# Kernel tuning notes

Measured on AMD Instinct MI355X. Metric: run time of the kernel, lower is better.

Reference implementation:

```python
import jax, jax.numpy as jnp
import numpy as np

N_NODES = 50000
N_EDGES = 800000
IN_DIM = 128
OUT_DIM = 128
NEG_INIT = -1e9  # matches torch fill_(-1e9) init for scatter amax
LEAKY_SLOPE = 0.01  # nn.LeakyReLU default


def setup_inputs() -> dict:
    key = jax.random.key(0)
    ks = jax.random.split(key, 8)
    x = jax.random.normal(ks[0], (N_NODES, IN_DIM), dtype=jnp.float32)
    edge_index = jax.random.randint(ks[1], (2, N_EDGES), 0, N_NODES, dtype=jnp.int64)
    edge_weight = jax.random.uniform(ks[2], (N_EDGES,), dtype=jnp.float32)
    # MLP params (nn.Linear default init: U(-1/sqrt(fan_in), 1/sqrt(fan_in)))
    s1 = 1.0 / np.sqrt(IN_DIM)
    s2 = 1.0 / np.sqrt(OUT_DIM)
    w1 = jax.random.uniform(ks[3], (OUT_DIM, IN_DIM), minval=-s1, maxval=s1, dtype=jnp.float32)
    b1 = jax.random.uniform(ks[4], (OUT_DIM,), minval=-s1, maxval=s1, dtype=jnp.float32)
    w2 = jax.random.uniform(ks[5], (OUT_DIM, OUT_DIM), minval=-s2, maxval=s2, dtype=jnp.float32)
    b2 = jax.random.uniform(ks[6], (OUT_DIM,), minval=-s2, maxval=s2, dtype=jnp.float32)
    eps = jnp.zeros((1,), dtype=jnp.float32)
    return {"x": x, "edge_index": edge_index, "edge_weight": edge_weight,
            "w1": w1, "b1": b1, "w2": w2, "b2": b2, "eps": eps}


def reference(x, edge_index, edge_weight, w1, b1, w2, b2, eps):
    src = edge_index[0]
    dst = edge_index[1]
    # gather + optional edge-weight scale: [E, D]
    messages = x[src] * edge_weight[:, None]
    # scatter-max to dst; init at -1e9 so include_self=False semantics hold
    agg = jnp.full(x.shape, NEG_INIT, dtype=x.dtype).at[dst].max(messages)
    agg = jnp.where(agg == NEG_INIT, jnp.zeros_like(agg), agg)  # isolated nodes -> 0
    h = (1.0 + eps) * x + agg  # eps broadcasts ([1])
    h = h @ w1.T + b1
    h = jnp.where(h >= 0, h, LEAKY_SLOPE * h)  # LeakyReLU
    out = h @ w2.T + b2
    return out
```

## Files before the change

kernel.cpp:

```cpp
#include <hip/hip_runtime.h>
#include <stdint.h>

#define NN 50000
#define NE 800000
#define D  128
#define CAP 64
#define OVF_CAP 131072

#define CNT_OFF     64
#define OVF_CNT_OFF (CNT_OFF + NN)
#define OVF_OFF     (OVF_CNT_OFF + 4)
#define BKT_OFF     312320
#define XH_OFF      (BKT_OFF + NN * CAP)
#define WH_OFF      (XH_OFF + 65536 * (D / 2))

#define HSTRIDE 136

#define FILL_BLKS 3125
#define PX_BLKS   6250
#define PW_BLKS   32

typedef _Float16 half8 __attribute__((ext_vector_type(8)));
typedef __attribute__((ext_vector_type(4))) float float4v;

__device__ __forceinline__ float b2f(uint16_t u) {
    union { uint32_t u; float f; } v; v.u = ((uint32_t)u) << 16; return v.f;
}
__device__ __forceinline__ uint16_t f2b(float f) {
    union { float f; uint32_t u; } v; v.f = f;
    uint32_t r = v.u + 0x7fffu + ((v.u >> 16) & 1u);
    return (uint16_t)(r >> 16);
}
__device__ __forceinline__ ushort f2h(float f) {
    union { _Float16 h; ushort u; } v; v.h = (_Float16)f; return v.u;
}
__device__ __forceinline__ float h2f(ushort u) {
    union { ushort u; _Float16 h; } v; v.u = u; return (float)v.h;
}

__device__ __forceinline__ void block_probe(const uint16_t* __restrict__ xraw,
                                            const int* __restrict__ eraw,
                                            int* sflags) {
    int t = threadIdx.x;
    if (t < 64) {
        float v0 = b2f(xraw[2 * t]);
        float v1 = b2f(xraw[2 * t + 1]);
        int bad = (!(v0 > -1e4f && v0 < 1e4f)) || (!(v1 > -1e4f && v1 < 1e4f));
        unsigned long long bm = __ballot(bad);
        int nz = (t < 32) ? (eraw[2 * t + 1] != 0) : 0;
        unsigned long long im = __ballot(nz);
        if (t == 0) { sflags[0] = bm ? 1 : 0; sflags[1] = im ? 0 : 1; }
    }
    __syncthreads();
}

__global__ __launch_bounds__(256) void prep_fill_kernel(
    const uint16_t* __restrict__ xraw,
    const int*      __restrict__ eraw,
    const uint16_t* __restrict__ ewraw,
    const uint16_t* __restrict__ w1raw,
    const uint16_t* __restrict__ w2raw,
    int* __restrict__ ws)
{
    __shared__ int sflags[2];
    block_probe(xraw, eraw, sflags);
    const int f32 = sflags[0], i64 = sflags[1];

    int bid = blockIdx.x;
    if (bid < FILL_BLKS) {
        int e = bid * 256 + threadIdx.x;
        int src, dst;
        if (i64) {
            const long long* e64 = (const long long*)eraw;
            src = (int)e64[e];
            dst = (int)e64[NE + e];
        } else {
            src = eraw[e];
            dst = eraw[NE + e];
        }
        if ((unsigned)src >= NN || (unsigned)dst >= NN) return;
        uint w = f32 ? (uint)f2h(((const float*)ewraw)[e]) : (uint)f2h(b2f(ewraw[e]));
        uint entry = (w << 16) | (uint)src;
        int slot = atomicAdd(ws + CNT_OFF + dst, 1) + 1;
        if (slot < CAP) {
            ((uint*)(ws + BKT_OFF))[(size_t)dst * CAP + slot] = entry;
        } else {
            int o = atomicAdd(ws + OVF_CNT_OFF, 1) + 1;
            if (o < OVF_CAP) {
                ws[OVF_OFF + 2 * o]     = dst;
                ws[OVF_OFF + 2 * o + 1] = (int)entry;
            }
        }
    } else if (bid < FILL_BLKS + PX_BLKS) {
        int i4 = ((bid - FILL_BLKS) * 256 + threadIdx.x) * 4;
        ushort* dst = (ushort*)(ws + XH_OFF);
        if (f32) {
            float4 v = *(const float4*)((const float*)xraw + i4);
            ushort4 o; o.x = f2h(v.x); o.y = f2h(v.y); o.z = f2h(v.z); o.w = f2h(v.w);
            *(ushort4*)(dst + i4) = o;
        } else {
            ushort4 v = *(const ushort4*)(xraw + i4);
            ushort4 o; o.x = f2h(b2f(v.x)); o.y = f2h(b2f(v.y));
            o.z = f2h(b2f(v.z)); o.w = f2h(b2f(v.w));
            *(ushort4*)(dst + i4) = o;
        }
    } else {
        int i4 = ((bid - FILL_BLKS - PX_BLKS) * 256 + threadIdx.x) * 4;
        const uint16_t* src = (i4 < 16384) ? w1raw : w2raw;
        int off = i4 & 16383;
        ushort* dst = (ushort*)(ws + WH_OFF);
        if (f32) {
            float4 v = *(const float4*)((const float*)src + off);
            ushort4 o; o.x = f2h(v.x); o.y = f2h(v.y); o.z = f2h(v.z); o.w = f2h(v.w);
            *(ushort4*)(dst + i4) = o;
        } else {
            ushort4 v = *(const ushort4*)(src + off);
            ushort4 o; o.x = f2h(b2f(v.x)); o.y = f2h(b2f(v.y));
            o.z = f2h(b2f(v.z)); o.w = f2h(b2f(v.w));
            *(ushort4*)(dst + i4) = o;
        }
    }
}

__global__ __launch_bounds__(256) void gmlp_kernel(
    const uint16_t* __restrict__ xraw,
    const int*      __restrict__ eraw,
    const uint16_t* __restrict__ b1raw,
    const uint16_t* __restrict__ b2raw,
    const uint16_t* __restrict__ epsraw,
    const int* __restrict__ ws,
    uint16_t* __restrict__ outraw)
{
    __shared__ int    sflags[2];
    __shared__ uint   tl[16 * (HSTRIDE / 2)];
    __shared__ ushort hl[16 * HSTRIDE];

    block_probe(xraw, eraw, sflags);
    const int f32 = sflags[0];

    const int tid  = threadIdx.x;
    const int wave = tid >> 6;
    const int lane = tid & 63;
    const int m    = lane & 15;
    const int quad = lane >> 4;
    const int node0 = blockIdx.x * 16;

    const ushort* w1h = (const ushort*)(ws + WH_OFF);
    const ushort* w2h = w1h + 16384;
    const uint*   xh  = (const uint*)(ws + XH_OFF);
    const uint*   bkt = (const uint*)(ws + BKT_OFF);
    const uint    lane4 = (uint)lane * 4;

    const float eps1 = 1.0f + (f32 ? ((const float*)epsraw)[0] : b2f(epsraw[0]));

    int cr[4];
    #pragma unroll
    for (int j = 0; j < 4; ++j)
        cr[j] = ws[CNT_OFF + node0 + wave * 4 + j];

    for (int j = 0; j < 4; ++j) {
        int nl = wave * 4 + j;
        int n  = node0 + nl;
        int deg = cr[j] + 1;
        int cnt = (deg < CAP) ? deg : CAP;

        uint mm[16];
        #pragma unroll
        for (int u = 0; u < 16; ++u) mm[u] = 0xFFFFFFFFu;

        const uint* brow = bkt + (size_t)n * CAP;
        for (int i = 0; i < cnt; i += 16) {
            uint4 q[4];
            #pragma unroll
            for (int qq = 0; qq < 4; ++qq) q[qq] = *(const uint4*)(brow + i + qq * 4);
            #pragma unroll
            for (int u = 0; u < 16; ++u) {
                uint e0  = ((const uint*)q)[u];
                uint off = ((e0 & 0xffffu) << 8) + lane4;
                uint v   = *(const uint*)((const char*)xh + off);
                uint p;
                asm("v_pk_mul_f16 %0, %1, %2 op_sel:[0,1] op_sel_hi:[1,1]"
                    : "=v"(p) : "v"(v), "v"(e0));
                asm("v_pk_max_f16 %0, %0, %1" : "+v"(mm[u]) : "v"(p));
            }
        }
        #pragma unroll
        for (int u = 8; u > 0; u >>= 1)
            #pragma unroll
            for (int v2 = 0; v2 < u; ++v2)
                asm("v_pk_max_f16 %0, %0, %1" : "+v"(mm[v2]) : "v"(mm[v2 + u]));

        float mx = h2f((ushort)(mm[0] & 0xffffu));
        float my = h2f((ushort)(mm[0] >> 16));

        if (deg > CAP) {
            int novf = ws[OVF_CNT_OFF] + 1;
            if (novf > OVF_CAP) novf = OVF_CAP;
            for (int o = 0; o < novf; ++o) {
                if (ws[OVF_OFF + 2 * o] == n) {
                    uint e0 = (uint)ws[OVF_OFF + 2 * o + 1];
                    uint v  = xh[(e0 & 0xffffu) * 64 + lane];
                    float w = h2f((ushort)(e0 >> 16));
                    mx = fmaxf(mx, h2f((ushort)(v & 0xffffu)) * w);
                    my = fmaxf(my, h2f((ushort)(v >> 16)) * w);
                }
            }
        }
        if (deg == 0) { mx = 0.f; my = 0.f; }

        uint xv = xh[(size_t)n * 64 + lane];
        float t0 = eps1 * h2f((ushort)(xv & 0xffffu)) + mx;
        float t1 = eps1 * h2f((ushort)(xv >> 16)) + my;
        tl[nl * (HSTRIDE / 2) + lane] = (uint)f2h(t0) | ((uint)f2h(t1) << 16);
    }
    __syncthreads();

    half8 a[4];
    {
        const ushort* arow = (const ushort*)tl + m * HSTRIDE + quad * 8;
        #pragma unroll
        for (int kb = 0; kb < 4; ++kb) a[kb] = *(const half8*)(arow + kb * 32);
    }

    #pragma unroll
    for (int t = 0; t < 2; ++t) {
        int ct = wave * 2 + t;
        float4v c = {0.f, 0.f, 0.f, 0.f};
        const ushort* brow = w1h + (size_t)(ct * 16 + m) * 128 + quad * 8;
        #pragma unroll
        for (int kb = 0; kb < 4; ++kb)
            c = __builtin_amdgcn_mfma_f32_16x16x32_f16(a[kb], *(const half8*)(brow + kb * 32), c, 0, 0, 0);
        float bias = f32 ? ((const float*)b1raw)[ct * 16 + m] : b2f(b1raw[ct * 16 + m]);
        #pragma unroll
        for (int r = 0; r < 4; ++r) {
            float v = c[r] + bias;
            v = (v >= 0.f) ? v : 0.01f * v;
            hl[(quad * 4 + r) * HSTRIDE + ct * 16 + m] = f2h(v);
        }
    }
    __syncthreads();

    half8 ah[4];
    {
        const ushort* hrow = hl + m * HSTRIDE + quad * 8;
        #pragma unroll
        for (int kb = 0; kb < 4; ++kb) ah[kb] = *(const half8*)(hrow + kb * 32);
    }

    #pragma unroll
    for (int t = 0; t < 2; ++t) {
        int ct = wave * 2 + t;
        float4v c = {0.f, 0.f, 0.f, 0.f};
        const ushort* brow = w2h + (size_t)(ct * 16 + m) * 128 + quad * 8;
        #pragma unroll
        for (int kb = 0; kb < 4; ++kb)
            c = __builtin_amdgcn_mfma_f32_16x16x32_f16(ah[kb], *(const half8*)(brow + kb * 32), c, 0, 0, 0);
        float bias = f32 ? ((const float*)b2raw)[ct * 16 + m] : b2f(b2raw[ct * 16 + m]);
        #pragma unroll
        for (int r = 0; r < 4; ++r) {
            float v = c[r] + bias;
            size_t o = (size_t)(node0 + quad * 4 + r) * 128 + ct * 16 + m;
            if (f32) ((float*)outraw)[o] = v;
            else     outraw[o] = f2b(v);
        }
    }
}

extern "C" void kernel_launch(void* const* d_in, const int* in_sizes, int n_in,
                              void* d_out, int out_size, void* d_ws, size_t ws_size,
                              hipStream_t stream) {
    const uint16_t* x    = (const uint16_t*)d_in[0];
    const int*      eidx = (const int*)     d_in[1];
    const uint16_t* ew   = (const uint16_t*)d_in[2];
    const uint16_t* w1   = (const uint16_t*)d_in[3];
    const uint16_t* b1   = (const uint16_t*)d_in[4];
    const uint16_t* w2   = (const uint16_t*)d_in[5];
    const uint16_t* b2   = (const uint16_t*)d_in[6];
    const uint16_t* eps  = (const uint16_t*)d_in[7];
    uint16_t*       out  = (uint16_t*)d_out;
    int* ws = (int*)d_ws;

    hipMemsetAsync((char*)d_ws + (size_t)CNT_OFF * 4, 0xFF,
                   (size_t)(BKT_OFF + (size_t)NN * CAP - CNT_OFF) * 4, stream);
    prep_fill_kernel<<<FILL_BLKS + PX_BLKS + PW_BLKS, 256, 0, stream>>>(
        x, eidx, ew, w1, w2, ws);
    gmlp_kernel<<<NN / 16, 256, 0, stream>>>(x, eidx, b1, b2, eps, ws, out);
}
```

Baseline: 195.5 us.

## Shrink workspace memset, batch edge atomics, interleave gathers across four nodes

The memset now clears only the per-node counters and overflow count instead of the whole bucket array. Bucket entries past each node's count are masked in the gather loop, so they no longer need the 0xFF fill. The fill stage now handles four edges per thread with the atomics issued back to back. The aggregation loop gathers bucket entries and x rows for all four nodes of a wave before reducing, which exposes more outstanding loads at the cost of higher register pressure.

```diff
diff --git a/kernel.cpp b/kernel.cpp
--- a/kernel.cpp
+++ b/kernel.cpp
@@ -16,7 +16,7 @@
 
 #define HSTRIDE 136
 
-#define FILL_BLKS 3125
+#define FILL_BLKS 782
 #define PX_BLKS   6250
 #define PW_BLKS   32
 
@@ -68,27 +68,44 @@
 
     int bid = blockIdx.x;
     if (bid < FILL_BLKS) {
-        int e = bid * 256 + threadIdx.x;
-        int src, dst;
-        if (i64) {
-            const long long* e64 = (const long long*)eraw;
-            src = (int)e64[e];
-            dst = (int)e64[NE + e];
-        } else {
-            src = eraw[e];
-            dst = eraw[NE + e];
-        }
-        if ((unsigned)src >= NN || (unsigned)dst >= NN) return;
-        uint w = f32 ? (uint)f2h(((const float*)ewraw)[e]) : (uint)f2h(b2f(ewraw[e]));
-        uint entry = (w << 16) | (uint)src;
-        int slot = atomicAdd(ws + CNT_OFF + dst, 1) + 1;
-        if (slot < CAP) {
-            ((uint*)(ws + BKT_OFF))[(size_t)dst * CAP + slot] = entry;
-        } else {
-            int o = atomicAdd(ws + OVF_CNT_OFF, 1) + 1;
-            if (o < OVF_CAP) {
-                ws[OVF_OFF + 2 * o]     = dst;
-                ws[OVF_OFF + 2 * o + 1] = (int)entry;
+        int ebase = bid * 1024 + threadIdx.x;
+        int dst[4]; uint ent[4]; bool val[4];
+        #pragma unroll
+        for (int k = 0; k < 4; ++k) {
+            int e  = ebase + k * 256;
+            val[k] = (e < NE);
+            int ec = val[k] ? e : 0;
+            int s, d2;
+            if (i64) {
+                const long long* e64 = (const long long*)eraw;
+                s  = (int)e64[ec];
+                d2 = (int)e64[NE + ec];
+            } else {
+                s  = eraw[ec];
+                d2 = eraw[NE + ec];
+            }
+            if ((unsigned)s >= NN || (unsigned)d2 >= NN) val[k] = false;
+            uint w = f32 ? (uint)f2h(((const float*)ewraw)[ec])
+                         : (uint)f2h(b2f(ewraw[ec]));
+            dst[k] = d2;
+            ent[k] = (w << 16) | (uint)(s & 0xffff);
+        }
+        int slot[4];
+        #pragma unroll
+        for (int k = 0; k < 4; ++k) {
+            slot[k] = 0x7fffffff;
+            if (val[k]) slot[k] = atomicAdd(ws + CNT_OFF + dst[k], 1) + 1;
+        }
+        #pragma unroll
+        for (int k = 0; k < 4; ++k) {
+            if (slot[k] < CAP) {
+                ((uint*)(ws + BKT_OFF))[(size_t)dst[k] * CAP + slot[k]] = ent[k];
+            } else if (slot[k] != 0x7fffffff) {
+                int o = atomicAdd(ws + OVF_CNT_OFF, 1) + 1;
+                if (o < OVF_CAP) {
+                    ws[OVF_OFF + 2 * o]     = dst[k];
+                    ws[OVF_OFF + 2 * o + 1] = (int)ent[k];
+                }
             }
         }
     } else if (bid < FILL_BLKS + PX_BLKS) {
@@ -148,52 +165,74 @@
     const ushort* w1h = (const ushort*)(ws + WH_OFF);
     const ushort* w2h = w1h + 16384;
     const uint*   xh  = (const uint*)(ws + XH_OFF);
+    const char*   xhb = (const char*)xh;
     const uint*   bkt = (const uint*)(ws + BKT_OFF);
     const uint    lane4 = (uint)lane * 4;
 
     const float eps1 = 1.0f + (f32 ? ((const float*)epsraw)[0] : b2f(epsraw[0]));
 
-    int cr[4];
+    int deg[4], cnt[4], itn[4];
     #pragma unroll
     for (int j = 0; j < 4; ++j)
-        cr[j] = ws[CNT_OFF + node0 + wave * 4 + j];
-
+        deg[j] = ws[CNT_OFF + node0 + wave * 4 + j] + 1;
+    #pragma unroll
+    for (int j = 0; j < 4; ++j) {
+        cnt[j] = (deg[j] < CAP) ? deg[j] : CAP;
+        itn[j] = (cnt[j] + 15) >> 4;
+    }
+
+    uint mm[4][4];
+    #pragma unroll
+    for (int j = 0; j < 4; ++j)
+        #pragma unroll
+        for (int c = 0; c < 4; ++c) mm[j][c] = 0xFFFFFFFFu;
+
+    for (int step = 0; step < 4; ++step) {
+        if (!((itn[0] > step) | (itn[1] > step) | (itn[2] > step) | (itn[3] > step)))
+            break;
+        uint qq[4][16];
+        uint vv[4][16];
+        #pragma unroll
+        for (int j = 0; j < 4; ++j) if (step < itn[j]) {
+            const uint* brow = bkt + (size_t)(node0 + wave * 4 + j) * CAP + step * 16;
+            #pragma unroll
+            for (int q4 = 0; q4 < 4; ++q4)
+                *(uint4*)&qq[j][q4 * 4] = *(const uint4*)(brow + q4 * 4);
+        }
+        #pragma unroll
+        for (int j = 0; j < 4; ++j) if (step < itn[j]) {
+            #pragma unroll
+            for (int u = 0; u < 16; ++u) {
+                uint off = ((qq[j][u] & 0xffffu) << 8) + lane4;
+                vv[j][u] = *(const uint*)(xhb + off);
+            }
+        }
+        #pragma unroll
+        for (int j = 0; j < 4; ++j) if (step < itn[j]) {
+            int cbase = step * 16;
+            #pragma unroll
+            for (int u = 0; u < 16; ++u) {
+                uint e0 = qq[j][u];
+                uint wb = ((cbase + u) < cnt[j]) ? e0 : 0xffffffffu;
+                uint p;
+                asm("v_pk_mul_f16 %0, %1, %2 op_sel:[0,1] op_sel_hi:[1,1]"
+                    : "=v"(p) : "v"(vv[j][u]), "v"(wb));
+                asm("v_pk_max_f16 %0, %0, %1" : "+v"(mm[j][u & 3]) : "v"(p));
+            }
+        }
+    }
+
+    #pragma unroll
     for (int j = 0; j < 4; ++j) {
         int nl = wave * 4 + j;
         int n  = node0 + nl;
-        int deg = cr[j] + 1;
-        int cnt = (deg < CAP) ? deg : CAP;
-
-        uint mm[16];
-        #pragma unroll
-        for (int u = 0; u < 16; ++u) mm[u] = 0xFFFFFFFFu;
-
-        const uint* brow = bkt + (size_t)n * CAP;
-        for (int i = 0; i < cnt; i += 16) {
-            uint4 q[4];
-            #pragma unroll
-            for (int qq = 0; qq < 4; ++qq) q[qq] = *(const uint4*)(brow + i + qq * 4);
-            #pragma unroll
-            for (int u = 0; u < 16; ++u) {
-                uint e0  = ((const uint*)q)[u];
-                uint off = ((e0 & 0xffffu) << 8) + lane4;
-                uint v   = *(const uint*)((const char*)xh + off);
-                uint p;
-                asm("v_pk_mul_f16 %0, %1, %2 op_sel:[0,1] op_sel_hi:[1,1]"
-                    : "=v"(p) : "v"(v), "v"(e0));
-                asm("v_pk_max_f16 %0, %0, %1" : "+v"(mm[u]) : "v"(p));
-            }
-        }
-        #pragma unroll
-        for (int u = 8; u > 0; u >>= 1)
-            #pragma unroll
-            for (int v2 = 0; v2 < u; ++v2)
-                asm("v_pk_max_f16 %0, %0, %1" : "+v"(mm[v2]) : "v"(mm[v2 + u]));
-
-        float mx = h2f((ushort)(mm[0] & 0xffffu));
-        float my = h2f((ushort)(mm[0] >> 16));
-
-        if (deg > CAP) {
+        asm("v_pk_max_f16 %0, %0, %1" : "+v"(mm[j][0]) : "v"(mm[j][1]));
+        asm("v_pk_max_f16 %0, %0, %1" : "+v"(mm[j][2]) : "v"(mm[j][3]));
+        asm("v_pk_max_f16 %0, %0, %1" : "+v"(mm[j][0]) : "v"(mm[j][2]));
+        float mx = h2f((ushort)(mm[j][0] & 0xffffu));
+        float my = h2f((ushort)(mm[j][0] >> 16));
+
+        if (deg[j] > CAP) {
             int novf = ws[OVF_CNT_OFF] + 1;
             if (novf > OVF_CAP) novf = OVF_CAP;
             for (int o = 0; o < novf; ++o) {
@@ -206,7 +245,7 @@
                 }
             }
         }
-        if (deg == 0) { mx = 0.f; my = 0.f; }
+        if (deg[j] == 0) { mx = 0.f; my = 0.f; }
 
         uint xv = xh[(size_t)n * 64 + lane];
         float t0 = eps1 * h2f((ushort)(xv & 0xffffu)) + mx;
@@ -281,7 +320,7 @@
     int* ws = (int*)d_ws;
 
     hipMemsetAsync((char*)d_ws + (size_t)CNT_OFF * 4, 0xFF,
-                   (size_t)(BKT_OFF + (size_t)NN * CAP - CNT_OFF) * 4, stream);
+                   (size_t)(NN + 1) * 4, stream);
     prep_fill_kernel<<<FILL_BLKS + PX_BLKS + PW_BLKS, 256, 0, stream>>>(
         x, eidx, ew, w1, w2, ws);
     gmlp_kernel<<<NN / 16, 256, 0, stream>>>(x, eidx, b1, b2, eps, ws, out);
```

Result: slower. 225.1 us (+15.1%).

## Shrink workspace memset, mask bucket tails, prefetch next node's bucket row

Applied to the files above, without the earlier changes.

Stops clearing the whole 12.8 MB bucket array to 0xFF each call and only resets the counters, because bucket slots past the count are now masked in-register (reads beyond the count load the padding entry 0xffffffff). It prefetches the first 16 bucket entries of the next node while the current node is being aggregated. It cuts the max accumulators from 16 to 4 to save registers, and sets launch_bounds to 8 blocks for higher occupancy. The risks are extra select instructions, a longer dependency chain on the 4 accumulators, and possible register spills under the tighter bound.

```diff
diff --git a/kernel.cpp b/kernel.cpp
--- a/kernel.cpp
+++ b/kernel.cpp
@@ -122,7 +122,7 @@
     }
 }
 
-__global__ __launch_bounds__(256) void gmlp_kernel(
+__global__ __launch_bounds__(256, 8) void gmlp_kernel(
     const uint16_t* __restrict__ xraw,
     const int*      __restrict__ eraw,
     const uint16_t* __restrict__ b1raw,
@@ -148,52 +148,79 @@
     const ushort* w1h = (const ushort*)(ws + WH_OFF);
     const ushort* w2h = w1h + 16384;
     const uint*   xh  = (const uint*)(ws + XH_OFF);
+    const char*   xhb = (const char*)xh;
     const uint*   bkt = (const uint*)(ws + BKT_OFF);
     const uint    lane4 = (uint)lane * 4;
 
     const float eps1 = 1.0f + (f32 ? ((const float*)epsraw)[0] : b2f(epsraw[0]));
 
-    int cr[4];
+    int deg[4], cnt[4];
     #pragma unroll
     for (int j = 0; j < 4; ++j)
-        cr[j] = ws[CNT_OFF + node0 + wave * 4 + j];
+        deg[j] = ws[CNT_OFF + node0 + wave * 4 + j] + 1;
+    #pragma unroll
+    for (int j = 0; j < 4; ++j)
+        cnt[j] = (deg[j] < CAP) ? deg[j] : CAP;
+
+    const uint* wbase = bkt + (size_t)(node0 + wave * 4) * CAP;
+
+    uint q[16];
+    #pragma unroll
+    for (int q4 = 0; q4 < 4; ++q4)
+        *(uint4*)&q[q4 * 4] = *(const uint4*)(wbase + q4 * 4);
 
     for (int j = 0; j < 4; ++j) {
         int nl = wave * 4 + j;
         int n  = node0 + nl;
-        int deg = cr[j] + 1;
-        int cnt = (deg < CAP) ? deg : CAP;
-
-        uint mm[16];
-        #pragma unroll
-        for (int u = 0; u < 16; ++u) mm[u] = 0xFFFFFFFFu;
-
-        const uint* brow = bkt + (size_t)n * CAP;
-        for (int i = 0; i < cnt; i += 16) {
-            uint4 q[4];
-            #pragma unroll
-            for (int qq = 0; qq < 4; ++qq) q[qq] = *(const uint4*)(brow + i + qq * 4);
+        const uint* brow = wbase + j * CAP;
+
+        uint mm[4];
+        #pragma unroll
+        for (int c = 0; c < 4; ++c) mm[c] = 0xFFFFFFFFu;
+
+        if (cnt[j] > 0) {
             #pragma unroll
             for (int u = 0; u < 16; ++u) {
-                uint e0  = ((const uint*)q)[u];
+                uint e0 = (u < cnt[j]) ? q[u] : 0xffffffffu;
                 uint off = ((e0 & 0xffffu) << 8) + lane4;
-                uint v   = *(const uint*)((const char*)xh + off);
+                uint v   = *(const uint*)(xhb + off);
                 uint p;
                 asm("v_pk_mul_f16 %0, %1, %2 op_sel:[0,1] op_sel_hi:[1,1]"
                     : "=v"(p) : "v"(v), "v"(e0));
-                asm("v_pk_max_f16 %0, %0, %1" : "+v"(mm[u]) : "v"(p));
+                asm("v_pk_max_f16 %0, %0, %1" : "+v"(mm[u & 3]) : "v"(p));
             }
         }
-        #pragma unroll
-        for (int u = 8; u > 0; u >>= 1)
+        for (int i = 16; i < cnt[j]; i += 16) {
+            uint q2[16];
             #pragma unroll
-            for (int v2 = 0; v2 < u; ++v2)
-                asm("v_pk_max_f16 %0, %0, %1" : "+v"(mm[v2]) : "v"(mm[v2 + u]));
-
+            for (int q4 = 0; q4 < 4; ++q4)
+                *(uint4*)&q2[q4 * 4] = *(const uint4*)(brow + i + q4 * 4);
+            #pragma unroll
+            for (int u = 0; u < 16; ++u) {
+                uint e0 = ((i + u) < cnt[j]) ? q2[u] : 0xffffffffu;
+                uint off = ((e0 & 0xffffu) << 8) + lane4;
+                uint v   = *(const uint*)(xhb + off);
+                uint p;
+                asm("v_pk_mul_f16 %0, %1, %2 op_sel:[0,1] op_sel_hi:[1,1]"
+                    : "=v"(p) : "v"(v), "v"(e0));
+                asm("v_pk_max_f16 %0, %0, %1" : "+v"(mm[u & 3]) : "v"(p));
+            }
+        }
+
+        if (j < 3) {
+            const uint* nb = brow + CAP;
+            #pragma unroll
+            for (int q4 = 0; q4 < 4; ++q4)
+                *(uint4*)&q[q4 * 4] = *(const uint4*)(nb + q4 * 4);
+        }
+
+        asm("v_pk_max_f16 %0, %0, %1" : "+v"(mm[0]) : "v"(mm[1]));
+        asm("v_pk_max_f16 %0, %0, %1" : "+v"(mm[2]) : "v"(mm[3]));
+        asm("v_pk_max_f16 %0, %0, %1" : "+v"(mm[0]) : "v"(mm[2]));
         float mx = h2f((ushort)(mm[0] & 0xffffu));
         float my = h2f((ushort)(mm[0] >> 16));
 
-        if (deg > CAP) {
+        if (deg[j] > CAP) {
             int novf = ws[OVF_CNT_OFF] + 1;
             if (novf > OVF_CAP) novf = OVF_CAP;
             for (int o = 0; o < novf; ++o) {
@@ -206,7 +233,7 @@
                 }
             }
         }
-        if (deg == 0) { mx = 0.f; my = 0.f; }
+        if (deg[j] == 0) { mx = 0.f; my = 0.f; }
 
         uint xv = xh[(size_t)n * 64 + lane];
         float t0 = eps1 * h2f((ushort)(xv & 0xffffu)) + mx;
@@ -281,7 +308,7 @@
     int* ws = (int*)d_ws;
 
     hipMemsetAsync((char*)d_ws + (size_t)CNT_OFF * 4, 0xFF,
-                   (size_t)(BKT_OFF + (size_t)NN * CAP - CNT_OFF) * 4, stream);
+                   (size_t)(NN + 1) * 4, stream);
     prep_fill_kernel<<<FILL_BLKS + PX_BLKS + PW_BLKS, 256, 0, stream>>>(
         x, eidx, ew, w1, w2, ws);
     gmlp_kernel<<<NN / 16, 256, 0, stream>>>(x, eidx, b1, b2, eps, ws, out);
```

New measurement: 204.5 us. 4.6% more time.
